# Kernel tuning notes

Hardware: AMD Instinct MI355X
Metric: run time of the kernel (lower is better)

The kernel has to match this reference:

```python
import jax, jax.numpy as jnp
import numpy as np

B, S, H = 2, 2048, 2048
NH, NKV, HD = 16, 4, 128
LAT = H // 8  # compression_ratio=8


def _rope_tables():
    inv_freq = 1.0 / (10000.0 ** (jnp.arange(0, HD, 2, dtype=jnp.float32) / HD))
    pos = jnp.arange(S, dtype=jnp.float32)
    freqs = pos[:, None] * inv_freq[None, :]          # [S, HD/2]
    emb = jnp.concatenate([freqs, freqs], axis=-1)    # [S, HD]
    return jnp.cos(emb)[None, None], jnp.sin(emb)[None, None]  # [1,1,S,HD]


def setup_inputs() -> dict:
    key = jax.random.key(0)
    ks = jax.random.split(key, 8)
    std = 0.02
    hidden_states = jax.random.normal(ks[0], (B, S, H), dtype=jnp.float32)
    cos, sin = _rope_tables()
    # additive causal mask, broadcast over batch/heads
    causal = jnp.tril(jnp.ones((S, S), dtype=bool))
    attention_mask = jnp.where(causal, 0.0, -1e9).astype(jnp.float32)[None, None]
    Wq = jax.random.normal(ks[1], (H, H), dtype=jnp.float32) * std
    Wk = jax.random.normal(ks[2], (NKV * HD, H), dtype=jnp.float32) * std
    Wv = jax.random.normal(ks[3], (NKV * HD, H), dtype=jnp.float32) * std
    Wo = jax.random.normal(ks[4], (H, H), dtype=jnp.float32) * std
    Wl_in = jax.random.normal(ks[5], (LAT, H), dtype=jnp.float32) * std
    Wl_out = jax.random.normal(ks[6], (H, LAT), dtype=jnp.float32) * std
    latent_gate = jnp.ones((1,), dtype=jnp.float32)
    return dict(hidden_states=hidden_states, cos=cos, sin=sin,
                attention_mask=attention_mask, Wq=Wq, Wk=Wk, Wv=Wv, Wo=Wo,
                Wl_in=Wl_in, Wl_out=Wl_out, latent_gate=latent_gate)


def _rotate_half(x):
    x1, x2 = jnp.split(x, 2, axis=-1)
    return jnp.concatenate([-x2, x1], axis=-1)


def reference(hidden_states, cos, sin, attention_mask, Wq, Wk, Wv, Wo,
              Wl_in, Wl_out, latent_gate):
    b, s, h = hidden_states.shape
    # projections (torch Linear: x @ W.T)
    q = (hidden_states @ Wq.T).reshape(b, s, NH, HD).transpose(0, 2, 1, 3)    # [b,nh,s,hd]
    k = (hidden_states @ Wk.T).reshape(b, s, NKV, HD).transpose(0, 2, 1, 3)   # [b,nkv,s,hd]
    v = (hidden_states @ Wv.T).reshape(b, s, NKV, HD).transpose(0, 2, 1, 3)
    # inline RoPE
    c, sn = cos[:, :, :s, :], sin[:, :, :s, :]
    q = q * c + _rotate_half(q) * sn
    k = k * c + _rotate_half(k) * sn
    # GQA: replicate kv heads (repeat_interleave along head dim)
    rep = NH // NKV
    k = jnp.repeat(k, rep, axis=1)
    v = jnp.repeat(v, rep, axis=1)
    scores = jnp.einsum('bhqd,bhkd->bhqk', q, k) / np.sqrt(HD).astype(np.float32)
    scores = scores + attention_mask
    attn = jax.nn.softmax(scores, axis=-1)
    ctx = jnp.einsum('bhqk,bhkd->bhqd', attn, v)          # [b,nh,s,hd]
    ctx = ctx.transpose(0, 2, 1, 3).reshape(b, s, h)
    attn_out = ctx @ Wo.T
    latent = (hidden_states @ Wl_in.T) @ Wl_out.T          # low-rank residual branch
    return attn_out + latent_gate * latent
```

## Files before the change

### kernel.cpp

```cpp
#include <hip/hip_runtime.h>
#include <hip/hip_bf16.h>

#define Bn   2
#define Sn   2048
#define Hn   2048
#define NHn  16
#define NKVn 4
#define HDn  128
#define LATn 256
#define Mn   (Bn*Sn)
#define KC   2304

typedef unsigned short ushort_t;
typedef __attribute__((ext_vector_type(8))) short bf16x8;
typedef __attribute__((ext_vector_type(8))) unsigned short ushort8;
typedef __attribute__((ext_vector_type(4))) float f32x4;

__device__ __forceinline__ ushort_t f2bf(float f) {
    unsigned u = __float_as_uint(f);
    u += 0x7fffu + ((u >> 16) & 1u);
    return (ushort_t)(u >> 16);
}
__device__ __forceinline__ float bf2f(ushort_t h) {
    return __uint_as_float(((unsigned)h) << 16);
}
__device__ __forceinline__ void async16(const void* g, void* l) {
    __builtin_amdgcn_global_load_lds(
        (__attribute__((address_space(1))) void*)g,
        (__attribute__((address_space(3))) void*)l, 16, 0, 0);
}

struct CastArgs {
    const float* src[7];
    ushort_t*    dst[7];
    int n4[7];
    int sshift[7];
    int dcols[7];
    int dcoff[7];
};
__global__ __launch_bounds__(256)
void cast_fused(CastArgs a)
{
    int off = blockIdx.x * 256 + threadIdx.x;
    int seg = 0;
    while (seg < 6 && off >= a.n4[seg]) { off -= a.n4[seg]; ++seg; }
    const int r = off >> a.sshift[seg];
    const int c = off & ((1 << a.sshift[seg]) - 1);
    float4 f = ((const float4*)a.src[seg])[off];
    ushort4 o;
    o.x = f2bf(f.x); o.y = f2bf(f.y); o.z = f2bf(f.z); o.w = f2bf(f.w);
    ((ushort4*)a.dst[seg])[(size_t)r * a.dcols[seg] + a.dcoff[seg] + c] = o;
}

#define GEMM_BK64_LOOP(Aptr, Astr, Wptr, Wstr, Kdim)                          \
    for (int k0 = 0; k0 < (Kdim); k0 += 64) {                                 \
        _Pragma("unroll")                                                     \
        for (int it = 0; it < 4; ++it)                                        \
            async16((Aptr) + (size_t)(m0 + it*32 + srow)*(Astr) + k0 + scol,  \
                    As + (it*256 + tid)*8);                                   \
        _Pragma("unroll")                                                     \
        for (int it = 0; it < 4; ++it)                                        \
            async16((Wptr) + (size_t)(n0 + it*32 + srow)*(Wstr) + k0 + scol,  \
                    Bsm + (it*256 + tid)*8);                                  \
        __syncthreads();                                                      \
        _Pragma("unroll")                                                     \
        for (int hf = 0; hf < 2; ++hf) {                                      \
            bf16x8 af[4], bfr[4];                                             \
            _Pragma("unroll")                                                 \
            for (int mi = 0; mi < 4; ++mi)                                    \
                af[mi] = *(const bf16x8*)(As + aoff[hf*4 + mi]);              \
            _Pragma("unroll")                                                 \
            for (int ni = 0; ni < 4; ++ni)                                    \
                bfr[ni] = *(const bf16x8*)(Bsm + boff[hf*4 + ni]);            \
            _Pragma("unroll")                                                 \
            for (int mi = 0; mi < 4; ++mi)                                    \
                _Pragma("unroll")                                             \
                for (int ni = 0; ni < 4; ++ni)                                \
                    acc[mi][ni] = __builtin_amdgcn_mfma_f32_16x16x32_bf16(    \
                        af[mi], bfr[ni], acc[mi][ni], 0, 0, 0);               \
        }                                                                     \
        __syncthreads();                                                      \
    }

#define GEMM_COMMON_DECLS                                                     \
    const int tid  = threadIdx.x;                                             \
    const int lane = tid & 63, w = tid >> 6;                                  \
    const int t = lane & 15, q = lane >> 4;                                   \
    const int wm = w & 1, wn = w >> 1;                                        \
    const int srow = tid >> 3;                                                \
    const int scol = ((tid & 7) ^ ((tid >> 3) & 7)) * 8;                      \
    int aoff[8], boff[8];                                                     \
    _Pragma("unroll")                                                         \
    for (int hf = 0; hf < 2; ++hf)                                            \
        _Pragma("unroll")                                                     \
        for (int i = 0; i < 4; ++i) {                                         \
            aoff[hf*4 + i] = (wm*64 + i*16 + t)*64 + (((hf*4 + q) ^ (t & 7)) << 3); \
            boff[hf*4 + i] = (wn*64 + i*16 + t)*64 + (((hf*4 + q) ^ (t & 7)) << 3); \
        }                                                                     \
    f32x4 acc[4][4];                                                          \
    _Pragma("unroll")                                                         \
    for (int i = 0; i < 4; ++i)                                               \
        _Pragma("unroll")                                                     \
        for (int j = 0; j < 4; ++j) acc[i][j] = (f32x4){0.f, 0.f, 0.f, 0.f};

__global__ __launch_bounds__(256)
void gemm_qkv(const ushort_t* __restrict__ A, const ushort_t* __restrict__ W,
              ushort_t* __restrict__ qo, ushort_t* __restrict__ ko,
              ushort_t* __restrict__ vo)
{
    __shared__ __align__(16) ushort_t smem[16384];
    ushort_t* As  = smem;
    ushort_t* Bsm = smem + 8192;

    const int m0 = blockIdx.y * 128, n0 = blockIdx.x * 128;
    GEMM_COMMON_DECLS
    GEMM_BK64_LOOP(A, Hn, W, Hn, Hn)

    const int bidx = m0 >> 11, s0 = m0 & (Sn - 1);

    if (n0 >= 2560) {
        const int head = (n0 - 2560) >> 7;
        ushort_t* T = smem;
        #pragma unroll
        for (int h2 = 0; h2 < 2; ++h2) {
            __syncthreads();
            if (wn == h2) {
                #pragma unroll
                for (int mi = 0; mi < 4; ++mi)
                    #pragma unroll
                    for (int ni = 0; ni < 4; ++ni)
                        #pragma unroll
                        for (int r = 0; r < 4; ++r)
                            T[(wm*64 + mi*16 + q*4 + r)*64 + ni*16 + t] =
                                f2bf(acc[mi][ni][r]);
            }
            __syncthreads();
            const int dl = tid >> 2, tseg = (tid & 3) * 32;
            const size_t base =
                ((size_t)(bidx*NKVn + head)*HDn + h2*64 + dl) * Sn + s0 + tseg;
            #pragma unroll
            for (int j0 = 0; j0 < 4; ++j0) {
                ushort8 pk;
                #pragma unroll
                for (int u = 0; u < 8; ++u) pk[u] = T[(tseg + j0*8 + u)*64 + dl];
                *(ushort8*)(vo + base + j0*8) = pk;
            }
        }
        return;
    }

    ushort_t* outp;
    int hh;
    if (n0 < 2048) { outp = qo; hh = n0 >> 7; }
    else           { outp = ko; hh = (n0 - 2048) >> 7; }
    const int nheads = (n0 < 2048) ? NHn : NKVn;
    const size_t hbase = (((size_t)(bidx*nheads + hh))*Sn + s0) * HDn;

    #pragma unroll
    for (int mi = 0; mi < 4; ++mi)
        #pragma unroll
        for (int r = 0; r < 4; ++r) {
            const int sl = wm*64 + mi*16 + q*4 + r;
            #pragma unroll
            for (int ni = 0; ni < 4; ++ni) {
                const int d = wn*64 + ni*16 + t;
                outp[hbase + (size_t)sl*HDn + d] = f2bf(acc[mi][ni][r]);
            }
        }
}

template<int EPI>
__global__ __launch_bounds__(256)
void gemm_main(const ushort_t* __restrict__ A, const ushort_t* __restrict__ W,
               float* __restrict__ outf, ushort_t* __restrict__ outb,
               const float* __restrict__ gatep,
               int N, int K, int Astride, int Wstride, int OS)
{
    __shared__ __align__(16) ushort_t smem[16384];
    ushort_t* As  = smem;
    ushort_t* Bsm = smem + 8192;

    const int m0 = blockIdx.y * 128, n0 = blockIdx.x * 128;
    GEMM_COMMON_DECLS
    GEMM_BK64_LOOP(A, Astride, W, Wstride, K)

    float gate = 1.f;
    if (EPI == 2) gate = gatep[0];

    #pragma unroll
    for (int mi = 0; mi < 4; ++mi)
        #pragma unroll
        for (int r = 0; r < 4; ++r) {
            const int m = m0 + wm*64 + mi*16 + q*4 + r;
            #pragma unroll
            for (int ni = 0; ni < 4; ++ni) {
                const int n = n0 + wn*64 + ni*16 + t;
                const float v = acc[mi][ni][r];
                if (EPI == 0)      outf[(size_t)m * N + n] = v;
                else if (EPI == 2) outb[(size_t)m * OS + n] = f2bf(gate * v);
            }
        }
}

__global__ __launch_bounds__(256)
void rope2_bf16(ushort_t* __restrict__ qx, ushort_t* __restrict__ kx,
                const float* __restrict__ cosb, const float* __restrict__ sinb)
{
    const int gid = blockIdx.x * 256 + threadIdx.x;
    const int row = gid >> 6, d = gid & 63;
    ushort_t* x; int r;
    if (row < Bn*NHn*Sn) { x = qx; r = row; }
    else                 { x = kx; r = row - Bn*NHn*Sn; }
    const int s = r & (Sn - 1);
    const float c0 = cosb[s*HDn + d],      c1 = cosb[s*HDn + d + 64];
    const float s0 = sinb[s*HDn + d],      s1 = sinb[s*HDn + d + 64];
    const size_t base = (size_t)r * HDn;
    const float x0 = bf2f(x[base + d]), x1 = bf2f(x[base + d + 64]);
    x[base + d]      = f2bf(x0*c0 - x1*s0);
    x[base + d + 64] = f2bf(x1*c1 + x0*s1);
}

__global__ __launch_bounds__(256)
void attn_mfma(const ushort_t* __restrict__ qg, const ushort_t* __restrict__ kg,
               const ushort_t* __restrict__ vtg, ushort_t* __restrict__ ctxb)
{
    __shared__ __align__(16) ushort_t Ks[8192];
    __shared__ __align__(16) ushort_t Vt[8192];
    __shared__ __align__(16) ushort_t Ps[4096];

    const int tid = threadIdx.x;
    const int w = tid >> 6, lane = tid & 63;
    const int t = lane & 15, q = lane >> 4;
    const int bh = blockIdx.y;
    const int b = bh >> 4, h = bh & 15;
    const int kvh = h >> 2;
    const ushort_t* qhead  = qg  + ((size_t)(b*NHn  + h  ))*Sn*HDn;
    const ushort_t* khead  = kg  + ((size_t)(b*NKVn + kvh))*Sn*HDn;
    const ushort_t* vthead = vtg + ((size_t)(b*NKVn + kvh))*HDn*Sn;

    const int ksr = tid >> 4;
    const int ksb = (tid & 15) ^ (ksr & 15);
    const int vtr = tid >> 3;
    const int vtb = (tid & 7) ^ (vtr & 7);

    int aqo[4], bko[16], vto[16], pso[16];
    #pragma unroll
    for (int ks = 0; ks < 4; ++ks)
        aqo[ks] = (w*16 + t)*128 + (((ks*4 + q) ^ t) << 3);
    #pragma unroll
    for (int nb = 0; nb < 4; ++nb)
        #pragma unroll
        for (int ks = 0; ks < 4; ++ks)
            bko[nb*4 + ks] = (nb*16 + t)*128 + (((ks*4 + q) ^ t) << 3);
    #pragma unroll
    for (int d2 = 0; d2 < 8; ++d2)
        #pragma unroll
        for (int ksp = 0; ksp < 2; ++ksp)
            vto[d2*2 + ksp] = (d2*16 + t)*64 + (((ksp*4 + q) ^ (t & 7)) << 3);
    #pragma unroll
    for (int nb = 0; nb < 4; ++nb)
        #pragma unroll
        for (int r = 0; r < 4; ++r) {
            const int row = q*4 + r;
            pso[nb*4 + r] = row*64 + (((nb*2 + (t >> 3)) ^ (row & 7)) << 3) + (t & 7);
        }

    const float cexp2 = 0.12751744737492532f;
    ushort_t* Pw = Ps + w*1024;
    const int apo0 = t*64 + ((q ^ (t & 7)) << 3);
    const int apo1 = t*64 + (((4 + q) ^ (t & 7)) << 3);

    for (int rep = 0; rep < 2; ++rep) {
        const int qt = rep ? (31 - (int)blockIdx.x) : (int)blockIdx.x;

        __syncthreads();
        #pragma unroll
        for (int it = 0; it < 4; ++it)
            async16(qhead + (size_t)(qt*64 + it*16 + ksr)*HDn + ksb*8,
                    Ks + it*2048 + tid*8);
        __syncthreads();
        bf16x8 aq[4];
        #pragma unroll
        for (int ks = 0; ks < 4; ++ks) aq[ks] = *(const bf16x8*)(Ks + aqo[ks]);
        __syncthreads();

        float l_lane[4] = {0.f, 0.f, 0.f, 0.f};
        f32x4 O[8];
        #pragma unroll
        for (int d2 = 0; d2 < 8; ++d2) O[d2] = (f32x4){0.f, 0.f, 0.f, 0.f};

        for (int kt = 0; kt <= qt; ++kt) {
            #pragma unroll
            for (int it = 0; it < 4; ++it)
                async16(khead + (size_t)(kt*64 + it*16 + ksr)*HDn + ksb*8,
                        Ks + it*2048 + tid*8);
            #pragma unroll
            for (int it = 0; it < 4; ++it)
                async16(vthead + (size_t)(it*32 + vtr)*Sn + kt*64 + vtb*8,
                        Vt + it*2048 + tid*8);
            __syncthreads();

            f32x4 sc[4];
            #pragma unroll
            for (int nb = 0; nb < 4; ++nb) {
                sc[nb] = (f32x4){0.f, 0.f, 0.f, 0.f};
                #pragma unroll
                for (int ks = 0; ks < 4; ++ks) {
                    bf16x8 bk = *(const bf16x8*)(Ks + bko[nb*4 + ks]);
                    sc[nb] = __builtin_amdgcn_mfma_f32_16x16x32_bf16(
                        aq[ks], bk, sc[nb], 0, 0, 0);
                }
            }

            float ps[4][4];
            if (kt == qt) {
                #pragma unroll
                for (int nb = 0; nb < 4; ++nb) {
                    const int kj = kt*64 + nb*16 + t;
                    #pragma unroll
                    for (int r = 0; r < 4; ++r) {
                        const int qi = qt*64 + w*16 + q*4 + r;
                        ps[nb][r] = (kj <= qi) ? exp2f(sc[nb][r]*cexp2) : 0.f;
                    }
                }
            } else {
                #pragma unroll
                for (int nb = 0; nb < 4; ++nb)
                    #pragma unroll
                    for (int r = 0; r < 4; ++r)
                        ps[nb][r] = exp2f(sc[nb][r]*cexp2);
            }
            #pragma unroll
            for (int nb = 0; nb < 4; ++nb)
                #pragma unroll
                for (int r = 0; r < 4; ++r) {
                    l_lane[r] += ps[nb][r];
                    Pw[pso[nb*4 + r]] = f2bf(ps[nb][r]);
                }

            bf16x8 ap0 = *(const bf16x8*)(Pw + apo0);
            bf16x8 ap1 = *(const bf16x8*)(Pw + apo1);
            #pragma unroll
            for (int d2 = 0; d2 < 8; ++d2) {
                bf16x8 bv0 = *(const bf16x8*)(Vt + vto[d2*2 + 0]);
                O[d2] = __builtin_amdgcn_mfma_f32_16x16x32_bf16(ap0, bv0, O[d2], 0, 0, 0);
                bf16x8 bv1 = *(const bf16x8*)(Vt + vto[d2*2 + 1]);
                O[d2] = __builtin_amdgcn_mfma_f32_16x16x32_bf16(ap1, bv1, O[d2], 0, 0, 0);
            }
            __syncthreads();
        }

        float linv[4];
        #pragma unroll
        for (int r = 0; r < 4; ++r) {
            float lr = l_lane[r];
            lr += __shfl_xor(lr, 1);
            lr += __shfl_xor(lr, 2);
            lr += __shfl_xor(lr, 4);
            lr += __shfl_xor(lr, 8);
            linv[r] = 1.f / lr;
        }
        #pragma unroll
        for (int d2 = 0; d2 < 8; ++d2)
            #pragma unroll
            for (int r = 0; r < 4; ++r) {
                const size_t addr =
                    ((size_t)(b*Sn + qt*64 + w*16 + q*4 + r))*KC + h*HDn + d2*16 + t;
                ctxb[addr] = f2bf(O[d2][r] * linv[r]);
            }
    }
}

extern "C" void kernel_launch(void* const* d_in, const int* in_sizes, int n_in,
                              void* d_out, int out_size, void* d_ws, size_t ws_size,
                              hipStream_t stream)
{
    const float* hs    = (const float*)d_in[0];
    const float* cosb  = (const float*)d_in[1];
    const float* sinb  = (const float*)d_in[2];
    const float* Wq    = (const float*)d_in[4];
    const float* Wk    = (const float*)d_in[5];
    const float* Wv    = (const float*)d_in[6];
    const float* Wo    = (const float*)d_in[7];
    const float* Wlin  = (const float*)d_in[8];
    const float* Wlout = (const float*)d_in[9];
    const float* gate  = (const float*)d_in[10];
    float* out = (float*)d_out;

    ushort_t* p = (ushort_t*)d_ws;
    ushort_t* hsb    = p;  p += 8388608;
    ushort_t* Wqkvb  = p;  p += 3072*2048;
    ushort_t* Wcomb  = p;  p += 2048*KC;
    ushort_t* Wlinb  = p;  p += 524288;
    ushort_t* qbb    = p;  p += 8388608;
    ushort_t* kbb    = p;  p += 2097152;
    ushort_t* vtb    = p;  p += 2097152;
    ushort_t* ctxc   = p;  p += (size_t)Mn*KC;

    const dim3 blk(256);

    {
        CastArgs ca;
        ca.src[0]=hs;    ca.dst[0]=hsb;                 ca.n4[0]=2097152; ca.sshift[0]=21; ca.dcols[0]=1<<21; ca.dcoff[0]=0;
        ca.src[1]=Wq;    ca.dst[1]=Wqkvb;               ca.n4[1]=1048576; ca.sshift[1]=20; ca.dcols[1]=1<<20; ca.dcoff[1]=0;
        ca.src[2]=Wk;    ca.dst[2]=Wqkvb + 2048*2048;   ca.n4[2]=262144;  ca.sshift[2]=18; ca.dcols[2]=1<<18; ca.dcoff[2]=0;
        ca.src[3]=Wv;    ca.dst[3]=Wqkvb + 2560*2048;   ca.n4[3]=262144;  ca.sshift[3]=18; ca.dcols[3]=1<<18; ca.dcoff[3]=0;
        ca.src[4]=Wlin;  ca.dst[4]=Wlinb;               ca.n4[4]=131072;  ca.sshift[4]=17; ca.dcols[4]=1<<17; ca.dcoff[4]=0;
        ca.src[5]=Wo;    ca.dst[5]=Wcomb;               ca.n4[5]=1048576; ca.sshift[5]=9;  ca.dcols[5]=576;   ca.dcoff[5]=0;
        ca.src[6]=Wlout; ca.dst[6]=Wcomb;               ca.n4[6]=131072;  ca.sshift[6]=6;  ca.dcols[6]=576;   ca.dcoff[6]=512;
        cast_fused<<<19456, blk, 0, stream>>>(ca);
    }

    gemm_qkv<<<dim3(24, 32), blk, 0, stream>>>(hsb, Wqkvb, qbb, kbb, vtb);

    rope2_bf16<<<((Bn*NHn*Sn + Bn*NKVn*Sn)*64)/256, blk, 0, stream>>>(qbb, kbb, cosb, sinb);

    gemm_main<2><<<dim3(2, 32), blk, 0, stream>>>(hsb, Wlinb, nullptr, ctxc + 2048,
                                                  gate, LATn, Hn, Hn, Hn, KC);

    attn_mfma<<<dim3(16, Bn*NHn), blk, 0, stream>>>(qbb, kbb, vtb, ctxc);

    gemm_main<0><<<dim3(16, 32), blk, 0, stream>>>(ctxc, Wcomb, out, nullptr,
                                                   nullptr, Hn, KC, KC, KC, 0);
}
```

Baseline: 390.5 us.

## Double-buffer GEMM and attention K loads, fuse latent-in projection into QKV GEMM

The GEMM main loop moves from a single-buffered BK=64 tile to a double-buffered BK=32 pipeline, so the global-to-LDS load of the next K slice overlaps the MFMAs on the current one. The attention kernel double-buffers K tiles and prefetches the next tile while computing scores. The Wl_in projection is appended to the QKV weight matrix and computed inside gemm_qkv, which removes a separate small launch. The trade-offs are more LDS for the extra K buffer in attention and a smaller k-step per barrier in the GEMMs.

New measurement: 397.6 us. No clear change (+1.8%).

```diff
diff --git a/kernel.cpp b/kernel.cpp
--- a/kernel.cpp
+++ b/kernel.cpp
@@ -10,6 +10,7 @@
 #define LATn 256
 #define Mn   (Bn*Sn)
 #define KC   2304
+#define NWn  3328
 
 typedef unsigned short ushort_t;
 typedef __attribute__((ext_vector_type(8))) short bf16x8;
@@ -52,71 +53,97 @@
     ((ushort4*)a.dst[seg])[(size_t)r * a.dcols[seg] + a.dcoff[seg] + c] = o;
 }
 
-#define GEMM_BK64_LOOP(Aptr, Astr, Wptr, Wstr, Kdim)                          \
-    for (int k0 = 0; k0 < (Kdim); k0 += 64) {                                 \
-        _Pragma("unroll")                                                     \
-        for (int it = 0; it < 4; ++it)                                        \
-            async16((Aptr) + (size_t)(m0 + it*32 + srow)*(Astr) + k0 + scol,  \
-                    As + (it*256 + tid)*8);                                   \
-        _Pragma("unroll")                                                     \
-        for (int it = 0; it < 4; ++it)                                        \
-            async16((Wptr) + (size_t)(n0 + it*32 + srow)*(Wstr) + k0 + scol,  \
-                    Bsm + (it*256 + tid)*8);                                  \
-        __syncthreads();                                                      \
-        _Pragma("unroll")                                                     \
-        for (int hf = 0; hf < 2; ++hf) {                                      \
-            bf16x8 af[4], bfr[4];                                             \
-            _Pragma("unroll")                                                 \
-            for (int mi = 0; mi < 4; ++mi)                                    \
-                af[mi] = *(const bf16x8*)(As + aoff[hf*4 + mi]);              \
-            _Pragma("unroll")                                                 \
-            for (int ni = 0; ni < 4; ++ni)                                    \
-                bfr[ni] = *(const bf16x8*)(Bsm + boff[hf*4 + ni]);            \
-            _Pragma("unroll")                                                 \
-            for (int mi = 0; mi < 4; ++mi)                                    \
-                _Pragma("unroll")                                             \
-                for (int ni = 0; ni < 4; ++ni)                                \
-                    acc[mi][ni] = __builtin_amdgcn_mfma_f32_16x16x32_bf16(    \
-                        af[mi], bfr[ni], acc[mi][ni], 0, 0, 0);               \
-        }                                                                     \
-        __syncthreads();                                                      \
-    }
-
 #define GEMM_COMMON_DECLS                                                     \
     const int tid  = threadIdx.x;                                             \
     const int lane = tid & 63, w = tid >> 6;                                  \
     const int t = lane & 15, q = lane >> 4;                                   \
     const int wm = w & 1, wn = w >> 1;                                        \
-    const int srow = tid >> 3;                                                \
-    const int scol = ((tid & 7) ^ ((tid >> 3) & 7)) * 8;                      \
-    int aoff[8], boff[8];                                                     \
+    const int srow = tid >> 2;                                                \
+    const int scol = ((tid & 3) ^ ((tid >> 2) & 3)) * 8;                      \
+    ushort_t* const As0 = smem;                                               \
+    ushort_t* const Bs0 = smem + 4096;                                        \
+    ushort_t* const As1 = smem + 8192;                                        \
+    ushort_t* const Bs1 = smem + 12288;                                       \
+    int aoff[4], boff[4];                                                     \
     _Pragma("unroll")                                                         \
-    for (int hf = 0; hf < 2; ++hf)                                            \
-        _Pragma("unroll")                                                     \
-        for (int i = 0; i < 4; ++i) {                                         \
-            aoff[hf*4 + i] = (wm*64 + i*16 + t)*64 + (((hf*4 + q) ^ (t & 7)) << 3); \
-            boff[hf*4 + i] = (wn*64 + i*16 + t)*64 + (((hf*4 + q) ^ (t & 7)) << 3); \
-        }                                                                     \
+    for (int i = 0; i < 4; ++i) {                                             \
+        aoff[i] = (wm*64 + i*16 + t)*32 + ((q ^ (t & 3)) << 3);               \
+        boff[i] = (wn*64 + i*16 + t)*32 + ((q ^ (t & 3)) << 3);               \
+    }                                                                         \
     f32x4 acc[4][4];                                                          \
     _Pragma("unroll")                                                         \
     for (int i = 0; i < 4; ++i)                                               \
         _Pragma("unroll")                                                     \
         for (int j = 0; j < 4; ++j) acc[i][j] = (f32x4){0.f, 0.f, 0.f, 0.f};
 
+#define STAGE32(Abuf, Bbuf, Aptr, Astr, Wptr, Wstr, kk)                       \
+    _Pragma("unroll")                                                         \
+    for (int it = 0; it < 2; ++it)                                            \
+        async16((Aptr) + (size_t)(m0 + it*64 + srow)*(Astr) + (kk) + scol,    \
+                (Abuf) + (it*256 + tid)*8);                                   \
+    _Pragma("unroll")                                                         \
+    for (int it = 0; it < 2; ++it)                                            \
+        async16((Wptr) + (size_t)(n0 + it*64 + srow)*(Wstr) + (kk) + scol,    \
+                (Bbuf) + (it*256 + tid)*8);
+
+#define COMPUTE32(Abuf, Bbuf)                                                 \
+    {                                                                         \
+        bf16x8 af[4], bfr[4];                                                 \
+        _Pragma("unroll")                                                     \
+        for (int i = 0; i < 4; ++i) af[i]  = *(const bf16x8*)((Abuf) + aoff[i]); \
+        _Pragma("unroll")                                                     \
+        for (int i = 0; i < 4; ++i) bfr[i] = *(const bf16x8*)((Bbuf) + boff[i]); \
+        _Pragma("unroll")                                                     \
+        for (int mi = 0; mi < 4; ++mi)                                        \
+            _Pragma("unroll")                                                 \
+            for (int ni = 0; ni < 4; ++ni)                                    \
+                acc[mi][ni] = __builtin_amdgcn_mfma_f32_16x16x32_bf16(        \
+                    af[mi], bfr[ni], acc[mi][ni], 0, 0, 0);                   \
+    }
+
+#define GEMM_BK32_PIPE(Aptr, Astr, Wptr, Wstr, Kdim)                          \
+    STAGE32(As0, Bs0, Aptr, Astr, Wptr, Wstr, 0)                              \
+    __syncthreads();                                                          \
+    for (int k0 = 0; k0 < (Kdim); k0 += 64) {                                 \
+        STAGE32(As1, Bs1, Aptr, Astr, Wptr, Wstr, k0 + 32)                    \
+        COMPUTE32(As0, Bs0)                                                   \
+        __syncthreads();                                                      \
+        if (k0 + 64 < (Kdim)) {                                               \
+            STAGE32(As0, Bs0, Aptr, Astr, Wptr, Wstr, k0 + 64)                \
+        }                                                                     \
+        COMPUTE32(As1, Bs1)                                                   \
+        __syncthreads();                                                      \
+    }
+
 __global__ __launch_bounds__(256)
 void gemm_qkv(const ushort_t* __restrict__ A, const ushort_t* __restrict__ W,
               ushort_t* __restrict__ qo, ushort_t* __restrict__ ko,
-              ushort_t* __restrict__ vo)
+              ushort_t* __restrict__ vo, ushort_t* __restrict__ ctxb,
+              const float* __restrict__ gatep)
 {
     __shared__ __align__(16) ushort_t smem[16384];
-    ushort_t* As  = smem;
-    ushort_t* Bsm = smem + 8192;
-
     const int m0 = blockIdx.y * 128, n0 = blockIdx.x * 128;
     GEMM_COMMON_DECLS
-    GEMM_BK64_LOOP(A, Hn, W, Hn, Hn)
+    GEMM_BK32_PIPE(A, Hn, W, Hn, Hn)
 
     const int bidx = m0 >> 11, s0 = m0 & (Sn - 1);
+
+    if (n0 >= 3072) {
+        const float gate = gatep[0];
+        const int c0 = 2048 + (n0 - 3072);
+        #pragma unroll
+        for (int mi = 0; mi < 4; ++mi)
+            #pragma unroll
+            for (int r = 0; r < 4; ++r) {
+                const int m = m0 + wm*64 + mi*16 + q*4 + r;
+                #pragma unroll
+                for (int ni = 0; ni < 4; ++ni) {
+                    const int n = c0 + wn*64 + ni*16 + t;
+                    ctxb[(size_t)m * KC + n] = f2bf(gate * acc[mi][ni][r]);
+                }
+            }
+        return;
+    }
 
     if (n0 >= 2560) {
         const int head = (n0 - 2560) >> 7;
@@ -169,23 +196,14 @@
         }
 }
 
-template<int EPI>
 __global__ __launch_bounds__(256)
-void gemm_main(const ushort_t* __restrict__ A, const ushort_t* __restrict__ W,
-               float* __restrict__ outf, ushort_t* __restrict__ outb,
-               const float* __restrict__ gatep,
-               int N, int K, int Astride, int Wstride, int OS)
+void gemm_out(const ushort_t* __restrict__ A, const ushort_t* __restrict__ W,
+              float* __restrict__ outf)
 {
     __shared__ __align__(16) ushort_t smem[16384];
-    ushort_t* As  = smem;
-    ushort_t* Bsm = smem + 8192;
-
     const int m0 = blockIdx.y * 128, n0 = blockIdx.x * 128;
     GEMM_COMMON_DECLS
-    GEMM_BK64_LOOP(A, Astride, W, Wstride, K)
-
-    float gate = 1.f;
-    if (EPI == 2) gate = gatep[0];
+    GEMM_BK32_PIPE(A, KC, W, KC, KC)
 
     #pragma unroll
     for (int mi = 0; mi < 4; ++mi)
@@ -195,9 +213,7 @@
             #pragma unroll
             for (int ni = 0; ni < 4; ++ni) {
                 const int n = n0 + wn*64 + ni*16 + t;
-                const float v = acc[mi][ni][r];
-                if (EPI == 0)      outf[(size_t)m * N + n] = v;
-                else if (EPI == 2) outb[(size_t)m * OS + n] = f2bf(gate * v);
+                outf[(size_t)m * Hn + n] = acc[mi][ni][r];
             }
         }
 }
@@ -224,7 +240,7 @@
 void attn_mfma(const ushort_t* __restrict__ qg, const ushort_t* __restrict__ kg,
                const ushort_t* __restrict__ vtg, ushort_t* __restrict__ ctxb)
 {
-    __shared__ __align__(16) ushort_t Ks[8192];
+    __shared__ __align__(16) ushort_t Ks[2][8192];
     __shared__ __align__(16) ushort_t Vt[8192];
     __shared__ __align__(16) ushort_t Ps[4096];
 
@@ -277,11 +293,17 @@
         #pragma unroll
         for (int it = 0; it < 4; ++it)
             async16(qhead + (size_t)(qt*64 + it*16 + ksr)*HDn + ksb*8,
-                    Ks + it*2048 + tid*8);
+                    Ks[0] + it*2048 + tid*8);
         __syncthreads();
         bf16x8 aq[4];
         #pragma unroll
-        for (int ks = 0; ks < 4; ++ks) aq[ks] = *(const bf16x8*)(Ks + aqo[ks]);
+        for (int ks = 0; ks < 4; ++ks) aq[ks] = *(const bf16x8*)(Ks[0] + aqo[ks]);
+        __syncthreads();
+
+        #pragma unroll
+        for (int it = 0; it < 4; ++it)
+            async16(khead + (size_t)(it*16 + ksr)*HDn + ksb*8,
+                    Ks[0] + it*2048 + tid*8);
         __syncthreads();
 
         float l_lane[4] = {0.f, 0.f, 0.f, 0.f};
@@ -290,15 +312,19 @@
         for (int d2 = 0; d2 < 8; ++d2) O[d2] = (f32x4){0.f, 0.f, 0.f, 0.f};
 
         for (int kt = 0; kt <= qt; ++kt) {
-            #pragma unroll
-            for (int it = 0; it < 4; ++it)
-                async16(khead + (size_t)(kt*64 + it*16 + ksr)*HDn + ksb*8,
-                        Ks + it*2048 + tid*8);
+            const ushort_t* Kc = Ks[kt & 1];
+            ushort_t*       Kn = Ks[(kt & 1) ^ 1];
+
             #pragma unroll
             for (int it = 0; it < 4; ++it)
                 async16(vthead + (size_t)(it*32 + vtr)*Sn + kt*64 + vtb*8,
                         Vt + it*2048 + tid*8);
-            __syncthreads();
+            if (kt < qt) {
+                #pragma unroll
+                for (int it = 0; it < 4; ++it)
+                    async16(khead + (size_t)((kt+1)*64 + it*16 + ksr)*HDn + ksb*8,
+                            Kn + it*2048 + tid*8);
+            }
 
             f32x4 sc[4];
             #pragma unroll
@@ -306,7 +332,7 @@
                 sc[nb] = (f32x4){0.f, 0.f, 0.f, 0.f};
                 #pragma unroll
                 for (int ks = 0; ks < 4; ++ks) {
-                    bf16x8 bk = *(const bf16x8*)(Ks + bko[nb*4 + ks]);
+                    bf16x8 bk = *(const bf16x8*)(Kc + bko[nb*4 + ks]);
                     sc[nb] = __builtin_amdgcn_mfma_f32_16x16x32_bf16(
                         aq[ks], bk, sc[nb], 0, 0, 0);
                 }
@@ -337,6 +363,8 @@
                     l_lane[r] += ps[nb][r];
                     Pw[pso[nb*4 + r]] = f2bf(ps[nb][r]);
                 }
+
+            __syncthreads();
 
             bf16x8 ap0 = *(const bf16x8*)(Pw + apo0);
             bf16x8 ap1 = *(const bf16x8*)(Pw + apo1);
@@ -389,9 +417,8 @@
 
     ushort_t* p = (ushort_t*)d_ws;
     ushort_t* hsb    = p;  p += 8388608;
-    ushort_t* Wqkvb  = p;  p += 3072*2048;
+    ushort_t* Wqkvb  = p;  p += (size_t)NWn*2048;
     ushort_t* Wcomb  = p;  p += 2048*KC;
-    ushort_t* Wlinb  = p;  p += 524288;
     ushort_t* qbb    = p;  p += 8388608;
     ushort_t* kbb    = p;  p += 2097152;
     ushort_t* vtb    = p;  p += 2097152;
@@ -405,21 +432,17 @@
         ca.src[1]=Wq;    ca.dst[1]=Wqkvb;               ca.n4[1]=1048576; ca.sshift[1]=20; ca.dcols[1]=1<<20; ca.dcoff[1]=0;
         ca.src[2]=Wk;    ca.dst[2]=Wqkvb + 2048*2048;   ca.n4[2]=262144;  ca.sshift[2]=18; ca.dcols[2]=1<<18; ca.dcoff[2]=0;
         ca.src[3]=Wv;    ca.dst[3]=Wqkvb + 2560*2048;   ca.n4[3]=262144;  ca.sshift[3]=18; ca.dcols[3]=1<<18; ca.dcoff[3]=0;
-        ca.src[4]=Wlin;  ca.dst[4]=Wlinb;               ca.n4[4]=131072;  ca.sshift[4]=17; ca.dcols[4]=1<<17; ca.dcoff[4]=0;
+        ca.src[4]=Wlin;  ca.dst[4]=Wqkvb + 3072*2048;   ca.n4[4]=131072;  ca.sshift[4]=17; ca.dcols[4]=1<<17; ca.dcoff[4]=0;
         ca.src[5]=Wo;    ca.dst[5]=Wcomb;               ca.n4[5]=1048576; ca.sshift[5]=9;  ca.dcols[5]=576;   ca.dcoff[5]=0;
         ca.src[6]=Wlout; ca.dst[6]=Wcomb;               ca.n4[6]=131072;  ca.sshift[6]=6;  ca.dcols[6]=576;   ca.dcoff[6]=512;
         cast_fused<<<19456, blk, 0, stream>>>(ca);
     }
 
-    gemm_qkv<<<dim3(24, 32), blk, 0, stream>>>(hsb, Wqkvb, qbb, kbb, vtb);
+    gemm_qkv<<<dim3(26, 32), blk, 0, stream>>>(hsb, Wqkvb, qbb, kbb, vtb, ctxc, gate);
 
     rope2_bf16<<<((Bn*NHn*Sn + Bn*NKVn*Sn)*64)/256, blk, 0, stream>>>(qbb, kbb, cosb, sinb);
 
-    gemm_main<2><<<dim3(2, 32), blk, 0, stream>>>(hsb, Wlinb, nullptr, ctxc + 2048,
-                                                  gate, LATn, Hn, Hn, Hn, KC);
-
     attn_mfma<<<dim3(16, Bn*NHn), blk, 0, stream>>>(qbb, kbb, vtb, ctxc);
 
-    gemm_main<0><<<dim3(16, 32), blk, 0, stream>>>(ctxc, Wcomb, out, nullptr,
-                                                   nullptr, Hn, KC, KC, KC, 0);
-}
+    gemm_out<<<dim3(16, 32), blk, 0, stream>>>(ctxc, Wcomb, out);
+}
```
